# Optimization experiments

Hardware: AMD Instinct MI355X
Metric: run time of the kernel (lower is better)

The kernel has to match this reference:

```python
import jax, jax.numpy as jnp
import numpy as np
from jax import lax

REG = 0.1
REG_M = 0.001
N_ITER = 250  # POT default numItermax=1000 with early stopping; 250 fixed iters converges here
EPS = 1e-8

N_TOK = 4096
D_EMB = 2048


def _xavier_uniform(key, shape):
    fan_in, fan_out = shape
    bound = float(np.sqrt(6.0 / (fan_in + fan_out)))
    return jax.random.uniform(key, shape, jnp.float32, -bound, bound)


def setup_inputs() -> dict:
    key = jax.random.key(0)
    kx, ky, kd = jax.random.split(key, 3)
    X = jax.random.normal(kx, (N_TOK, D_EMB), jnp.float32)
    Y = jax.random.normal(ky, (N_TOK, D_EMB), jnp.float32)
    delta_ot = _xavier_uniform(kd, (N_TOK, N_TOK))
    return {"X": X, "Y": Y, "delta_ot": delta_ot}


def pairwise_cosine(X, Y):
    Xn = X / jnp.maximum(jnp.linalg.norm(X, axis=-1, keepdims=True), EPS)
    Yn = Y / jnp.maximum(jnp.linalg.norm(Y, axis=-1, keepdims=True), EPS)
    return Xn @ Yn.T  # [n, m]


def sinkhorn_unbalanced(M, reg, reg_m, n_iter):
    # POT ot.unbalanced.sinkhorn_unbalanced, KL-relaxed marginals, scaling form.
    n, m = M.shape
    a = jnp.full((n,), 1.0 / n, M.dtype)
    b = jnp.full((m,), 1.0 / m, M.dtype)
    K = jnp.exp(-M / reg)  # [n, m]
    fi = reg_m / (reg_m + reg)

    def step(carry, _):
        u, v = carry
        u = (a / (K @ v)) ** fi
        v = (b / (K.T @ u)) ** fi
        return (u, v), None

    (u, v), _ = lax.scan(step, (jnp.ones((n,), M.dtype), jnp.ones((m,), M.dtype)), None, length=n_iter)
    return u[:, None] * K * v[None, :]


def reference(X, Y, delta_ot):
    A = pairwise_cosine(X, Y)                      # [n, m]
    # OT weight computed on detached sim (sim.data in torch) -> stop_gradient
    M = -lax.stop_gradient(A)
    W = sinkhorn_unbalanced(M, REG, REG_M, N_ITER)  # [n, m], no grad
    T = A * W + delta_ot                            # [n, m]
    X_aligned = T @ X                               # [n, d] (requires m == n)
    return X_aligned
```

## Files before the change

### kernel.cpp

```cpp
#include <hip/hip_runtime.h>
#include <stdint.h>


typedef __attribute__((ext_vector_type(8))) __bf16 bf16x8;
typedef __attribute__((ext_vector_type(4))) float f32x4;
typedef __attribute__((ext_vector_type(16))) float f32x16;
typedef __attribute__((ext_vector_type(8))) unsigned short ushort8;

#define N_TOK 4096
#define D_EMB 2048
#define FI 0.009900990099009901f
#define LOG2A (-12.0f)

__device__ __forceinline__ unsigned short f2bf(float f) {
  union { float f; uint32_t u; } c; c.f = f;
  uint32_t r = (c.u + 0x7FFFu + ((c.u >> 16) & 1u)) >> 16;
  return (unsigned short)r;
}
__device__ __forceinline__ float bf2f(unsigned short h) {
  union { uint32_t u; float f; } c; c.u = ((uint32_t)h) << 16;
  return c.f;
}
__device__ __forceinline__ float pow_fi_of(float s) {
  return exp2f(FI * (LOG2A - log2f(s)));
}

typedef const __attribute__((address_space(1))) unsigned int* as1_u32p;
typedef __attribute__((address_space(3))) unsigned int* as3_u32p;
__device__ __forceinline__ void gload16(const void* g, void* l) {
  __builtin_amdgcn_global_load_lds((as1_u32p)g, (as3_u32p)l, 16, 0, 0);
}

__global__ __launch_bounds__(256) void rownorm_all(
    const float* __restrict__ X, const float* __restrict__ Y,
    unsigned short* __restrict__ Xn, unsigned short* __restrict__ Yn) {
  const int row = blockIdx.x & 4095;
  const int isY = blockIdx.x >> 12;
  const int t = threadIdx.x;
  const float* r = (isY ? Y : X) + (size_t)row * D_EMB;
  float4 a = *(const float4*)(r + t * 8);
  float4 b = *(const float4*)(r + t * 8 + 4);
  float s = a.x * a.x + a.y * a.y + a.z * a.z + a.w * a.w
          + b.x * b.x + b.y * b.y + b.z * b.z + b.w * b.w;
#pragma unroll
  for (int off = 32; off; off >>= 1) s += __shfl_xor(s, off);
  __shared__ float wsum[4];
  if ((t & 63) == 0) wsum[t >> 6] = s;
  __syncthreads();
  float tot = wsum[0] + wsum[1] + wsum[2] + wsum[3];
  float scale = 1.0f / fmaxf(sqrtf(tot), 1e-8f);
  ushort8 o;
  o[0] = f2bf(a.x * scale); o[1] = f2bf(a.y * scale);
  o[2] = f2bf(a.z * scale); o[3] = f2bf(a.w * scale);
  o[4] = f2bf(b.x * scale); o[5] = f2bf(b.y * scale);
  o[6] = f2bf(b.z * scale); o[7] = f2bf(b.w * scale);
  unsigned short* outn = isY ? Yn : Xn;
  *(ushort8*)(outn + (size_t)row * D_EMB + t * 8) = o;
}

__global__ __launch_bounds__(256) void transpose_f32_to_bf16(
    const float* __restrict__ in, unsigned short* __restrict__ out, int R, int C) {
  __shared__ float tile[32][33];
  const int bi = blockIdx.y * 32, bj = blockIdx.x * 32;
  const int tx = threadIdx.x, ty = threadIdx.y;
#pragma unroll
  for (int dy = 0; dy < 32; dy += 8)
    tile[ty + dy][tx] = in[(size_t)(bi + ty + dy) * C + bj + tx];
  __syncthreads();
#pragma unroll
  for (int dy = 0; dy < 32; dy += 8)
    out[(size_t)(bj + ty + dy) * R + bi + tx] = f2bf(tile[tx][ty + dy]);
}

__global__ __launch_bounds__(256, 1) void gemm256w4(
    const unsigned short* __restrict__ Amat, const unsigned short* __restrict__ Bmat,
    int ldA, int ldB, int nt, int ldC,
    unsigned short* __restrict__ outKbf, float* __restrict__ rsum,
    float* __restrict__ csum) {
  __shared__ alignas(16) char smem[131072];
  const int t = threadIdx.x;
  const int l = t & 63;
  const int w = t >> 6;

  const int nwg = gridDim.x * gridDim.y;
  const int lin = blockIdx.y * gridDim.x + blockIdx.x;
  const int lin2 = (lin & 7) * (nwg >> 3) + (lin >> 3);
  const int bx = lin2 % gridDim.x;
  const int by = lin2 / gridDim.x;
  const int bM = by * 256;
  const int bN = bx * 256;
  const int wrow = w >> 1;
  const int wcol = w & 1;

  const unsigned short* Ag = Amat + (size_t)bM * ldA;
  const unsigned short* Bg = Bmat + (size_t)bN * ldB;

  const int st_row = w * 64 + (l >> 3);
  const int st_col = ((l & 7) ^ (l >> 3)) * 8;
  const int st_lds = w * 8192;

  const int rsw0 = (((l >> 4) + 0) ^ (l & 7)) * 16;
  const int rsw1 = (((l >> 4) + 4) ^ (l & 7)) * 16;
  const int arow = l & 15;

  auto stageA = [&](int k) {
    char* base = smem + (k & 1) * 32768 + st_lds;
    const unsigned short* g = Ag + (size_t)st_row * ldA + k * 64 + st_col;
#pragma unroll
    for (int i = 0; i < 8; ++i)
      gload16(g + (size_t)(i * 8) * ldA, base + i * 1024);
  };
  auto stageB = [&](int k) {
    char* base = smem + 65536 + (k & 1) * 32768 + st_lds;
    const unsigned short* g = Bg + (size_t)st_row * ldB + k * 64 + st_col;
#pragma unroll
    for (int i = 0; i < 8; ++i)
      gload16(g + (size_t)(i * 8) * ldB, base + i * 1024);
  };

  f32x4 acc[8][8] = {};

  stageA(0); stageB(0);
  __syncthreads();

  for (int k = 0; k < nt; ++k) {
    char* Abase = smem + (k & 1) * 32768;
    char* Bbase = smem + 65536 + (k & 1) * 32768;
    if (k + 1 < nt) { stageA(k + 1); stageB(k + 1); }

#pragma unroll
    for (int kk = 0; kk < 2; ++kk) {
      const int rsw = kk ? rsw1 : rsw0;
      bf16x8 af[8], bf[8];
#pragma unroll
      for (int m = 0; m < 8; ++m)
        af[m] = *(const bf16x8*)(Abase + (wrow * 128 + m * 16 + arow) * 128 + rsw);
#pragma unroll
      for (int n = 0; n < 8; ++n)
        bf[n] = *(const bf16x8*)(Bbase + (wcol * 128 + n * 16 + arow) * 128 + rsw);
#pragma unroll
      for (int m = 0; m < 8; ++m)
#pragma unroll
        for (int n = 0; n < 8; ++n)
          acc[m][n] = __builtin_amdgcn_mfma_f32_16x16x32_bf16(af[m], bf[n], acc[m][n], 0, 0, 0);
    }

    __syncthreads();
  }

  float cs[8] = {};
#pragma unroll
  for (int m = 0; m < 8; ++m) {
#pragma unroll
    for (int r = 0; r < 4; ++r) {
      const int i = bM + wrow * 128 + m * 16 + (l >> 4) * 4 + r;
      float rs = 0.0f;
#pragma unroll
      for (int n = 0; n < 8; ++n) {
        const int j = bN + wcol * 128 + n * 16 + (l & 15);
        const float kvf = __expf(10.0f * acc[m][n][r]);
        outKbf[(size_t)i * ldC + j] = f2bf(kvf);
        rs += kvf;
        cs[n] += kvf;
      }
      rs += __shfl_xor(rs, 1); rs += __shfl_xor(rs, 2);
      rs += __shfl_xor(rs, 4); rs += __shfl_xor(rs, 8);
      if ((l & 15) == 0) unsafeAtomicAdd(&rsum[i], rs);
    }
  }
#pragma unroll
  for (int n = 0; n < 8; ++n) {
    float c = cs[n];
    c += __shfl_xor(c, 16); c += __shfl_xor(c, 32);
    if (l < 16) {
      const int j = bN + wcol * 128 + n * 16 + l;
      unsafeAtomicAdd(&csum[j], c);
    }
  }
}

__global__ __launch_bounds__(256, 1) void gemm_t2(
    const unsigned short* __restrict__ Amat, const unsigned short* __restrict__ Bmat,
    int ldA, int ldB, int nt, int ldC, float* __restrict__ outC) {
  __shared__ alignas(16) char smem[98304];
  const int t = threadIdx.x;
  const int l = t & 63;
  const int w = t >> 6;

  const int nwg = gridDim.x * gridDim.y;
  const int lin = blockIdx.y * gridDim.x + blockIdx.x;
  const int lin2 = (lin & 7) * (nwg >> 3) + (lin >> 3);
  const int bx = lin2 % gridDim.x;
  const int by = lin2 / gridDim.x;
  const int bM = by * 256;
  const int bN = bx * 128;
  const int wrow = w >> 1;
  const int wcol = w & 1;

  const unsigned short* Ag = Amat + (size_t)bM * ldA;
  const unsigned short* Bg = Bmat + (size_t)bN * ldB;

  const int stA_row = w * 64 + (l >> 3);
  const int st_col = ((l & 7) ^ (l >> 3)) * 8;
  const int stA_lds = w * 8192;
  const int stB_row = w * 32 + (l >> 3);
  const int stB_lds = w * 4096;

  const int frow = l & 31;
  const int kg = l >> 5;
  const int xr = l & 7;

  auto stageA = [&](int k) {
    char* base = smem + (k & 1) * 32768 + stA_lds;
    const unsigned short* g = Ag + (size_t)stA_row * ldA + k * 64 + st_col;
#pragma unroll
    for (int i = 0; i < 8; ++i)
      gload16(g + (size_t)(i * 8) * ldA, base + i * 1024);
  };
  auto stageB = [&](int k) {
    char* base = smem + 65536 + (k & 1) * 16384 + stB_lds;
    const unsigned short* g = Bg + (size_t)stB_row * ldB + k * 64 + st_col;
#pragma unroll
    for (int i = 0; i < 4; ++i)
      gload16(g + (size_t)(i * 8) * ldB, base + i * 1024);
  };

  f32x16 acc[4][2] = {};

  stageA(0); stageB(0);
  __syncthreads();

  for (int k = 0; k < nt; ++k) {
    char* Abase = smem + (k & 1) * 32768;
    char* Bbase = smem + 65536 + (k & 1) * 16384;
    if (k + 1 < nt) { stageA(k + 1); stageB(k + 1); }

    bf16x8 aA[4], bA[2], aB[4], bB[2];
    auto LD = [&](int kk, bf16x8 (&af)[4], bf16x8 (&bf)[2]) {
      const int rsw = ((2 * kk + kg) ^ xr) * 16;
#pragma unroll
      for (int m = 0; m < 4; ++m)
        af[m] = *(const bf16x8*)(Abase + (wrow * 128 + m * 32 + frow) * 128 + rsw);
#pragma unroll
      for (int n = 0; n < 2; ++n)
        bf[n] = *(const bf16x8*)(Bbase + (wcol * 64 + n * 32 + frow) * 128 + rsw);
    };
    auto MM = [&](bf16x8 (&af)[4], bf16x8 (&bf)[2]) {
#pragma unroll
      for (int m = 0; m < 4; ++m)
#pragma unroll
        for (int n = 0; n < 2; ++n)
          acc[m][n] = __builtin_amdgcn_mfma_f32_32x32x16_bf16(af[m], bf[n], acc[m][n], 0, 0, 0);
    };
    LD(0, aA, bA);
    LD(1, aB, bB);
    MM(aA, bA);
    LD(2, aA, bA);
    MM(aB, bB);
    LD(3, aB, bB);
    MM(aA, bA);
    MM(aB, bB);

    __syncthreads();
  }

#pragma unroll
  for (int m = 0; m < 4; ++m)
#pragma unroll
    for (int n = 0; n < 2; ++n)
#pragma unroll
      for (int r = 0; r < 16; ++r) {
        const int i = bM + wrow * 128 + m * 32 + (r & 3) + 8 * (r >> 2) + 4 * kg;
        const int j = bN + wcol * 64 + n * 32 + frow;
        outC[(size_t)i * ldC + j] = acc[m][n][r];
      }
}

__global__ __launch_bounds__(256) void zero_small(float* p) {
  p[blockIdx.x * 256 + threadIdx.x] = 0.0f;
}

__global__ __launch_bounds__(256) void build_T(
    const unsigned short* __restrict__ Kbf,
    const float* __restrict__ delta, const float* __restrict__ rsum,
    const float* __restrict__ csum, unsigned short* __restrict__ Tbf) {
  const size_t e = ((size_t)blockIdx.x * 256 + threadIdx.x) * 8;
  const int i = (int)(e >> 12);
  const int j = (int)(e & 4095);
  const float ui = pow_fi_of(rsum[i]);
  ushort8 kv = *(const ushort8*)(Kbf + e);
  float4 d0 = *(const float4*)(delta + e);
  float4 d1 = *(const float4*)(delta + e + 4);
  float4 t0 = *(const float4*)(csum + j);
  float4 t1 = *(const float4*)(csum + j + 4);
  float v0x = pow_fi_of(t0.x), v0y = pow_fi_of(t0.y), v0z = pow_fi_of(t0.z), v0w = pow_fi_of(t0.w);
  float v1x = pow_fi_of(t1.x), v1y = pow_fi_of(t1.y), v1z = pow_fi_of(t1.z), v1w = pow_fi_of(t1.w);
  ushort8 o;
  float k0 = bf2f(kv[0]), k1 = bf2f(kv[1]), k2 = bf2f(kv[2]), k3 = bf2f(kv[3]);
  float k4 = bf2f(kv[4]), k5 = bf2f(kv[5]), k6 = bf2f(kv[6]), k7 = bf2f(kv[7]);
  o[0] = f2bf(0.1f * __logf(k0) * (ui * k0 * v0x) + d0.x);
  o[1] = f2bf(0.1f * __logf(k1) * (ui * k1 * v0y) + d0.y);
  o[2] = f2bf(0.1f * __logf(k2) * (ui * k2 * v0z) + d0.z);
  o[3] = f2bf(0.1f * __logf(k3) * (ui * k3 * v0w) + d0.w);
  o[4] = f2bf(0.1f * __logf(k4) * (ui * k4 * v1x) + d1.x);
  o[5] = f2bf(0.1f * __logf(k5) * (ui * k5 * v1y) + d1.y);
  o[6] = f2bf(0.1f * __logf(k6) * (ui * k6 * v1z) + d1.z);
  o[7] = f2bf(0.1f * __logf(k7) * (ui * k7 * v1w) + d1.w);
  *(ushort8*)(Tbf + e) = o;
}

extern "C" void kernel_launch(void* const* d_in, const int* in_sizes, int n_in,
                              void* d_out, int out_size, void* d_ws, size_t ws_size,
                              hipStream_t stream) {
  const float* X = (const float*)d_in[0];
  const float* Y = (const float*)d_in[1];
  const float* delta = (const float*)d_in[2];
  float* out = (float*)d_out;
  uint8_t* ws = (uint8_t*)d_ws;

  const size_t SZ_NN_BF = (size_t)N_TOK * N_TOK * 2;
  const size_t SZ_ND_BF = (size_t)N_TOK * D_EMB * 2;

  unsigned short* K_bf = (unsigned short*)(ws);
  unsigned short* T_bf = (unsigned short*)(ws + SZ_NN_BF);
  unsigned short* Xn = (unsigned short*)(ws + 2 * SZ_NN_BF);
  unsigned short* XT = Xn;
  float* rsum = (float*)(ws + 2 * SZ_NN_BF + SZ_ND_BF);
  float* csum = rsum + N_TOK;
  unsigned short* Yn = (unsigned short*)d_out;

  zero_small<<<32, 256, 0, stream>>>(rsum);
  rownorm_all<<<2 * N_TOK, 256, 0, stream>>>(X, Y, Xn, Yn);
  gemm256w4<<<dim3(16, 16, 1), 256, 0, stream>>>(
      Xn, Yn, D_EMB, D_EMB, D_EMB / 64, N_TOK, K_bf, rsum, csum);
  transpose_f32_to_bf16<<<dim3(D_EMB / 32, N_TOK / 32), dim3(32, 8), 0, stream>>>(
      X, XT, N_TOK, D_EMB);
  build_T<<<(N_TOK / 8) * (N_TOK / 256), 256, 0, stream>>>(K_bf, delta, rsum, csum, T_bf);
  gemm_t2<<<dim3(16, 16, 1), 256, 0, stream>>>(
      T_bf, XT, N_TOK, N_TOK, N_TOK / 64, D_EMB, out);
}
```

Measured before the change: 198.4 us.

## Fuse X cast and transpose, defer cosine normalization to GEMM epilogue

Replaces the separate row-normalize and transpose kernels with prep_x, which reads X once and emits row-major bf16, transposed bf16, and per-row sum of squares. Y is cast to bf16 unnormalized with its inverse norm stored separately. The GEMM epilogue applies both inverse norms before the exponent. This removes one full pass over X, at the cost of low-parallelism prep_x blocks with serialized sync loops and an extra workspace buffer.

```diff
diff --git a/kernel.cpp b/kernel.cpp
--- a/kernel.cpp
+++ b/kernel.cpp
@@ -6,6 +6,7 @@
 typedef __attribute__((ext_vector_type(4))) float f32x4;
 typedef __attribute__((ext_vector_type(16))) float f32x16;
 typedef __attribute__((ext_vector_type(8))) unsigned short ushort8;
+typedef __attribute__((ext_vector_type(4))) unsigned short ushort4v;
 
 #define N_TOK 4096
 #define D_EMB 2048
@@ -31,13 +32,12 @@
   __builtin_amdgcn_global_load_lds((as1_u32p)g, (as3_u32p)l, 16, 0, 0);
 }
 
-__global__ __launch_bounds__(256) void rownorm_all(
-    const float* __restrict__ X, const float* __restrict__ Y,
-    unsigned short* __restrict__ Xn, unsigned short* __restrict__ Yn) {
-  const int row = blockIdx.x & 4095;
-  const int isY = blockIdx.x >> 12;
+__global__ __launch_bounds__(256) void prep_y(
+    const float* __restrict__ Y, unsigned short* __restrict__ Yb,
+    float* __restrict__ sy) {
+  const int row = blockIdx.x;
   const int t = threadIdx.x;
-  const float* r = (isY ? Y : X) + (size_t)row * D_EMB;
+  const float* r = Y + (size_t)row * D_EMB;
   float4 a = *(const float4*)(r + t * 8);
   float4 b = *(const float4*)(r + t * 8 + 4);
   float s = a.x * a.x + a.y * a.y + a.z * a.z + a.w * a.w
@@ -48,35 +48,51 @@
   if ((t & 63) == 0) wsum[t >> 6] = s;
   __syncthreads();
   float tot = wsum[0] + wsum[1] + wsum[2] + wsum[3];
-  float scale = 1.0f / fmaxf(sqrtf(tot), 1e-8f);
   ushort8 o;
-  o[0] = f2bf(a.x * scale); o[1] = f2bf(a.y * scale);
-  o[2] = f2bf(a.z * scale); o[3] = f2bf(a.w * scale);
-  o[4] = f2bf(b.x * scale); o[5] = f2bf(b.y * scale);
-  o[6] = f2bf(b.z * scale); o[7] = f2bf(b.w * scale);
-  unsigned short* outn = isY ? Yn : Xn;
-  *(ushort8*)(outn + (size_t)row * D_EMB + t * 8) = o;
-}
-
-__global__ __launch_bounds__(256) void transpose_f32_to_bf16(
-    const float* __restrict__ in, unsigned short* __restrict__ out, int R, int C) {
+  o[0] = f2bf(a.x); o[1] = f2bf(a.y); o[2] = f2bf(a.z); o[3] = f2bf(a.w);
+  o[4] = f2bf(b.x); o[5] = f2bf(b.y); o[6] = f2bf(b.z); o[7] = f2bf(b.w);
+  *(ushort8*)(Yb + (size_t)row * D_EMB + t * 8) = o;
+  if (t == 0) sy[row] = 1.0f / fmaxf(sqrtf(tot), 1e-8f);
+}
+
+__global__ __launch_bounds__(256) void prep_x(
+    const float* __restrict__ X, unsigned short* __restrict__ Xb,
+    unsigned short* __restrict__ XTb, float* __restrict__ ssx) {
   __shared__ float tile[32][33];
-  const int bi = blockIdx.y * 32, bj = blockIdx.x * 32;
-  const int tx = threadIdx.x, ty = threadIdx.y;
-#pragma unroll
-  for (int dy = 0; dy < 32; dy += 8)
-    tile[ty + dy][tx] = in[(size_t)(bi + ty + dy) * C + bj + tx];
-  __syncthreads();
-#pragma unroll
-  for (int dy = 0; dy < 32; dy += 8)
-    out[(size_t)(bj + ty + dy) * R + bi + tx] = f2bf(tile[tx][ty + dy]);
+  const int r0 = blockIdx.y * 32;
+  const int c0 = blockIdx.x * 1024;
+  const int t = threadIdx.x;
+  const int row = t >> 3;
+  const int cg = (t & 7) * 4;
+  float ss = 0.0f;
+  for (int ct = 0; ct < 1024; ct += 32) {
+    const size_t gi = (size_t)(r0 + row) * D_EMB + c0 + ct + cg;
+    float4 v = *(const float4*)(X + gi);
+    ss += v.x * v.x + v.y * v.y + v.z * v.z + v.w * v.w;
+    ushort4v xo;
+    xo[0] = f2bf(v.x); xo[1] = f2bf(v.y); xo[2] = f2bf(v.z); xo[3] = f2bf(v.w);
+    *(ushort4v*)(Xb + gi) = xo;
+    tile[row][cg + 0] = v.x; tile[row][cg + 1] = v.y;
+    tile[row][cg + 2] = v.z; tile[row][cg + 3] = v.w;
+    __syncthreads();
+    const int dd = t >> 3;
+    const int rr = (t & 7) * 4;
+    ushort4v o;
+#pragma unroll
+    for (int e = 0; e < 4; ++e) o[e] = f2bf(tile[rr + e][dd]);
+    *(ushort4v*)(XTb + (size_t)(c0 + ct + dd) * N_TOK + r0 + rr) = o;
+    __syncthreads();
+  }
+  ss += __shfl_xor(ss, 1); ss += __shfl_xor(ss, 2); ss += __shfl_xor(ss, 4);
+  if ((t & 7) == 0) unsafeAtomicAdd(&ssx[r0 + row], ss);
 }
 
 __global__ __launch_bounds__(256, 1) void gemm256w4(
     const unsigned short* __restrict__ Amat, const unsigned short* __restrict__ Bmat,
     int ldA, int ldB, int nt, int ldC,
     unsigned short* __restrict__ outKbf, float* __restrict__ rsum,
-    float* __restrict__ csum) {
+    float* __restrict__ csum, const float* __restrict__ ssx,
+    const float* __restrict__ sy) {
   __shared__ alignas(16) char smem[131072];
   const int t = threadIdx.x;
   const int l = t & 63;
@@ -148,17 +164,22 @@
     __syncthreads();
   }
 
+  float syv[8];
+#pragma unroll
+  for (int n = 0; n < 8; ++n)
+    syv[n] = sy[bN + wcol * 128 + n * 16 + (l & 15)];
   float cs[8] = {};
 #pragma unroll
   for (int m = 0; m < 8; ++m) {
 #pragma unroll
     for (int r = 0; r < 4; ++r) {
       const int i = bM + wrow * 128 + m * 16 + (l >> 4) * 4 + r;
+      const float sxv = 1.0f / fmaxf(sqrtf(ssx[i]), 1e-8f);
       float rs = 0.0f;
 #pragma unroll
       for (int n = 0; n < 8; ++n) {
         const int j = bN + wcol * 128 + n * 16 + (l & 15);
-        const float kvf = __expf(10.0f * acc[m][n][r]);
+        const float kvf = __expf(10.0f * acc[m][n][r] * sxv * syv[n]);
         outKbf[(size_t)i * ldC + j] = f2bf(kvf);
         rs += kvf;
         cs[n] += kvf;
@@ -323,19 +344,20 @@
 
   unsigned short* K_bf = (unsigned short*)(ws);
   unsigned short* T_bf = (unsigned short*)(ws + SZ_NN_BF);
-  unsigned short* Xn = (unsigned short*)(ws + 2 * SZ_NN_BF);
-  unsigned short* XT = Xn;
-  float* rsum = (float*)(ws + 2 * SZ_NN_BF + SZ_ND_BF);
+  unsigned short* Xb = (unsigned short*)(ws + 2 * SZ_NN_BF);
+  unsigned short* XTb = (unsigned short*)(ws + 2 * SZ_NN_BF + SZ_ND_BF);
+  float* rsum = (float*)(ws + 2 * SZ_NN_BF + 2 * SZ_ND_BF);
   float* csum = rsum + N_TOK;
-  unsigned short* Yn = (unsigned short*)d_out;
-
-  zero_small<<<32, 256, 0, stream>>>(rsum);
-  rownorm_all<<<2 * N_TOK, 256, 0, stream>>>(X, Y, Xn, Yn);
+  float* ssx = csum + N_TOK;
+  float* sy = ssx + N_TOK;
+  unsigned short* Yb = (unsigned short*)d_out;
+
+  zero_small<<<48, 256, 0, stream>>>(rsum);
+  prep_y<<<N_TOK, 256, 0, stream>>>(Y, Yb, sy);
+  prep_x<<<dim3(2, 128), 256, 0, stream>>>(X, Xb, XTb, ssx);
   gemm256w4<<<dim3(16, 16, 1), 256, 0, stream>>>(
-      Xn, Yn, D_EMB, D_EMB, D_EMB / 64, N_TOK, K_bf, rsum, csum);
-  transpose_f32_to_bf16<<<dim3(D_EMB / 32, N_TOK / 32), dim3(32, 8), 0, stream>>>(
-      X, XT, N_TOK, D_EMB);
+      Xb, Yb, D_EMB, D_EMB, D_EMB / 64, N_TOK, K_bf, rsum, csum, ssx, sy);
   build_T<<<(N_TOK / 8) * (N_TOK / 256), 256, 0, stream>>>(K_bf, delta, rsum, csum, T_bf);
   gemm_t2<<<dim3(16, 16, 1), 256, 0, stream>>>(
-      T_bf, XT, N_TOK, N_TOK, N_TOK / 64, D_EMB, out);
-}
+      T_bf, XTb, N_TOK, N_TOK, N_TOK / 64, D_EMB, out);
+}
```

New measurement: 225.0 us. 1.13x slower.
